# Kernel tuning notes

Measured on AMD Instinct MI355X. Metric: run time of the kernel, lower is better.

## Reference

```python
import jax, jax.numpy as jnp
import numpy as np

N = 50000      # num_nodes
E = 800000     # num_edges
F_IN = 128     # node_features
H = 128        # hidden_channels
EPS = 1e-5     # BatchNorm eps


def setup_inputs() -> dict:
    key = jax.random.key(0)
    ks = jax.random.split(key, 6)
    x = jax.random.normal(ks[0], (N, F_IN), dtype=jnp.float32)
    edge_index = jax.random.randint(ks[1], (2, E), 0, N, dtype=jnp.int64)
    s = 0.05
    return {
        "x": x,
        "edge_index": edge_index,
        "g_in": jnp.ones((F_IN,), jnp.float32),
        "be_in": jnp.zeros((F_IN,), jnp.float32),
        "w1": jax.random.normal(ks[2], (F_IN, 2 * H), jnp.float32) * s,
        "b1": jnp.zeros((2 * H,), jnp.float32),
        "g1": jnp.ones((2 * H,), jnp.float32),
        "be1": jnp.zeros((2 * H,), jnp.float32),
        "w2": jax.random.normal(ks[3], (2 * H, H), jnp.float32) * s,
        "b2": jnp.zeros((H,), jnp.float32),
        "g2": jnp.ones((H,), jnp.float32),
        "be2": jnp.zeros((H,), jnp.float32),
    }


def batchnorm(x, g, b):
    # training-mode BatchNorm1d: batch stats over the node dimension (biased var)
    m = jnp.mean(x, axis=0)
    v = jnp.var(x, axis=0)
    return (x - m) * jax.lax.rsqrt(v + EPS) * g + b


def gcn_conv(x, w, b, src, dst, deg_inv_sqrt):
    # PyG GCNConv: transform, then D^{-1/2}(A+I)D^{-1/2} aggregation, then bias
    h = x @ w                                   # [N, out]
    norm = deg_inv_sqrt[src] * deg_inv_sqrt[dst]  # [E+N]
    msg = h[src] * norm[:, None]                # gather + scale
    out = jax.ops.segment_sum(msg, dst, num_segments=N)  # scatter-add
    return out + b


def reference(x, edge_index, g_in, be_in, w1, b1, g1, be1, w2, b2, g2, be2):
    # add self-loops once
    loop = jnp.arange(N, dtype=edge_index.dtype)
    src = jnp.concatenate([edge_index[0], loop])
    dst = jnp.concatenate([edge_index[1], loop])
    deg = jax.ops.segment_sum(jnp.ones_like(src, dtype=x.dtype), dst, num_segments=N)
    deg_inv_sqrt = jnp.where(deg > 0, jax.lax.rsqrt(jnp.maximum(deg, 1.0)), 0.0)

    h = batchnorm(x, g_in, be_in)
    # layer 1: F_IN -> 2H (no residual: shapes differ); dropout is identity in eval
    h = jax.nn.relu(batchnorm(gcn_conv(h, w1, b1, src, dst, deg_inv_sqrt), g1, be1))
    # layer 2 (final): 2H -> H
    h = jax.nn.relu(batchnorm(gcn_conv(h, w2, b2, src, dst, deg_inv_sqrt), g2, be2))
    return h
```

## Files before the change

kernel.cpp:

```cpp
#include <hip/hip_runtime.h>
#include <hip/hip_bf16.h>

#define NN 50000
#define NE 800000
#define FIN 128
#define HC1 256
#define HC2 128
#define EPSV 1e-5f
#define NTILE 196
#define CAP 8448
#define FILLMAX (CAP - 3840)
#define NQ 12500
#define CELL 56

typedef __attribute__((ext_vector_type(8))) short bf8;
typedef __attribute__((ext_vector_type(16))) float f32x16;

union BF8U { bf8 v; ushort u[8]; uint4 q; };

__device__ __forceinline__ float bf2f(ushort u) {
    union { uint i; float f; } c; c.i = ((uint)u) << 16; return c.f;
}
__device__ __forceinline__ float ulo(uint u) {
    union { uint i; float f; } c; c.i = u << 16; return c.f;
}
__device__ __forceinline__ float uhi(uint u) {
    union { uint i; float f; } c; c.i = u & 0xffff0000u; return c.f;
}
__device__ __forceinline__ ushort f2bf(float f) {
    return __builtin_bit_cast(ushort, __float2bfloat16(f));
}

__global__ void k_init(float* __restrict__ stats, uint* __restrict__ s0row) {
    int i = blockIdx.x * blockDim.x + threadIdx.x;
    if (i < 1024) stats[i] = 0.0f;
    if (i < 64) s0row[i] = 0u;
}

#define BKB NTILE
#define SB 391
#define WB 128

__device__ __forceinline__ void wprep_body(const float* __restrict__ W, ushort* __restrict__ wp,
                                           int idx, int K, int NC) {
    int j = idx & 7;
    int lane = (idx >> 3) & 63;
    int ts = idx >> 9;
    int KS = K / 16;
    int s = ts % KS;
    int t = ts / KS;
    int n = t * 32 + (lane & 31);
    int k = s * 16 + (lane >> 5) * 8 + j;
    wp[idx] = f2bf(W[(size_t)k * NC + n]);
}

__global__ __launch_bounds__(256) void k_bucket(
    const int* __restrict__ ei, int* __restrict__ gcnt, uint* __restrict__ cellbuf,
    const float* __restrict__ x, float* __restrict__ sum, float* __restrict__ sumsq,
    const float* __restrict__ w1, ushort* __restrict__ wp1,
    const float* __restrict__ w2, ushort* __restrict__ wp2) {
    int b = blockIdx.x;
    int t = threadIdx.x;
    if (b < BKB) {
        __shared__ int hist[256];
        __shared__ int sscan[256];
        __shared__ int offs[256];
        __shared__ int lcur[256];
        __shared__ uint stage[4096];
        hist[t] = 0;
        __syncthreads();
        int e0 = b * 4096;
        int total = min(4096, NE - e0);
        uint eu[16];
#pragma unroll
        for (int i = 0; i < 16; ++i) {
            int e = e0 + i * 256 + t;
            if (e < NE) {
                int s = ei[e];
                int d = ei[NE + e];
                s = min(max(s, 0), NN - 1);
                d = min(max(d, 0), NN - 1);
                int tile = d >> 8;
                eu[i] = ((uint)tile << 24) | ((uint)s << 8) | (uint)(d & 255);
                atomicAdd(&hist[tile], 1);
            } else eu[i] = 0xffffffffu;
        }
        __syncthreads();
        int h = hist[t];
        sscan[t] = h;
        __syncthreads();
#pragma unroll
        for (int off = 1; off < 256; off <<= 1) {
            int v = (t >= off) ? sscan[t - off] : 0;
            __syncthreads();
            sscan[t] += v;
            __syncthreads();
        }
        int excl = sscan[t] - h;
        offs[t] = excl;
        lcur[t] = excl;
        __syncthreads();
#pragma unroll
        for (int i = 0; i < 16; ++i) {
            if (eu[i] != 0xffffffffu) {
                int tile = eu[i] >> 24;
                int p = atomicAdd(&lcur[tile], 1);
                stage[p] = eu[i];
            }
        }
        __syncthreads();
        for (int p = t; p < total; p += 256) {
            uint u = stage[p];
            int T = u >> 24;
            int idx = p - offs[T];
            if (idx < CELL) cellbuf[(size_t)T * (BKB * CELL) + b * CELL + idx] = u;
        }
        if (t < NTILE) gcnt[t * BKB + b] = hist[t];
        return;
    }
    if (b < BKB + SB) {
        const int F4 = 32, RIF = 8, RPB = 128;
        int c4 = t & 31;
        int ro = t >> 5;
        int r0 = (b - BKB) * RPB;
        int r1 = min(r0 + RPB, NN);
        float4 s = make_float4(0.f, 0.f, 0.f, 0.f);
        float4 q = make_float4(0.f, 0.f, 0.f, 0.f);
        for (int r = r0 + ro; r < r1; r += RIF) {
            float4 v = ((const float4*)x)[(size_t)r * F4 + c4];
            s.x += v.x; s.y += v.y; s.z += v.z; s.w += v.w;
            q.x += v.x * v.x; q.y += v.y * v.y; q.z += v.z * v.z; q.w += v.w * v.w;
        }
        __shared__ float4 sS[256];
        __shared__ float4 sQ[256];
        sS[t] = s; sQ[t] = q;
        __syncthreads();
#pragma unroll
        for (int st = 128; st >= 32; st >>= 1) {
            if (t < st) {
                float4 a = sS[t + st], bb = sQ[t + st];
                sS[t].x += a.x; sS[t].y += a.y; sS[t].z += a.z; sS[t].w += a.w;
                sQ[t].x += bb.x; sQ[t].y += bb.y; sQ[t].z += bb.z; sQ[t].w += bb.w;
            }
            __syncthreads();
        }
        if (t < 32) {
            float4 a = sS[t], bb = sQ[t];
            atomicAdd(&sum[t * 4 + 0], a.x); atomicAdd(&sum[t * 4 + 1], a.y);
            atomicAdd(&sum[t * 4 + 2], a.z); atomicAdd(&sum[t * 4 + 3], a.w);
            atomicAdd(&sumsq[t * 4 + 0], bb.x); atomicAdd(&sumsq[t * 4 + 1], bb.y);
            atomicAdd(&sumsq[t * 4 + 2], bb.z); atomicAdd(&sumsq[t * 4 + 3], bb.w);
        }
        return;
    }
    if (b < BKB + SB + WB) {
        wprep_body(w1, wp1, (b - BKB - SB) * 256 + t, FIN, HC1);
        return;
    }
    wprep_body(w2, wp2, (b - BKB - SB - WB) * 256 + t, HC1, HC2);
}

__global__ __launch_bounds__(256) void k_csr(
    const int* __restrict__ gcnt, const uint* __restrict__ cellbuf,
    ushort* __restrict__ csr, int* __restrict__ cnt, int* __restrict__ rowstart,
    const float* __restrict__ sumIn, const float* __restrict__ sqIn,
    const float* __restrict__ g, const float* __restrict__ be,
    const float* __restrict__ x, ushort* __restrict__ s0) {
    __shared__ uint ubuf[CAP];
    __shared__ int ccnt[256];
    __shared__ int cscan[256];
    __shared__ int cnt256[256];
    __shared__ int scan[256];
    __shared__ int offs256[256];
    __shared__ int cur256[256];
    __shared__ int dcnt[256];
    __shared__ float ssc[128];
    __shared__ float ssh[128];
    int t = threadIdx.x;
    int tile = blockIdx.x;
    int t0 = tile << 8;
    if (t < 128) {
        float mean = sumIn[t] / (float)NN;
        float var = fmaxf(sqIn[t] / (float)NN - mean * mean, 0.f);
        float s = g[t] * rsqrtf(var + EPSV);
        ssc[t] = s;
        ssh[t] = be[t] - mean * s;
    }
    int cb = (t < BKB) ? min(gcnt[tile * BKB + t], CELL) : 0;
    ccnt[t] = cb;
    cnt256[t] = 0;
    cscan[t] = cb;
    __syncthreads();
#pragma unroll
    for (int off = 1; off < 256; off <<= 1) {
        int v = (t >= off) ? cscan[t - off] : 0;
        __syncthreads();
        cscan[t] += v;
        __syncthreads();
    }
    int size = min(cscan[255], FILLMAX);
    int cexcl = cscan[t] - cb;
    for (int i = 0; i < cb; ++i) {
        int w = cexcl + i;
        if (w < size) {
            uint u = cellbuf[(size_t)tile * (BKB * CELL) + t * CELL + i] & 0x00ffffffu;
            ubuf[w] = u;
            atomicAdd(&cnt256[u & 255u], 1);
        }
    }
    __syncthreads();
    int c = cnt256[t];
    dcnt[t] = c;
    int padded = (c + 15) & ~15;
    scan[t] = padded;
    __syncthreads();
#pragma unroll
    for (int off = 1; off < 256; off <<= 1) {
        int v = (t >= off) ? scan[t - off] : 0;
        __syncthreads();
        scan[t] += v;
        __syncthreads();
    }
    int excl = scan[t] - padded;
    offs256[t] = excl;
    cur256[t] = 0;
    int r = t0 + t;
    if (r < NN) {
        cnt[r] = c;
        rowstart[r] = tile * CAP + excl;
    }
    __syncthreads();
    for (int i = t; i < size; i += 256) {
        uint u = ubuf[i];
        int l = u & 255u;
        int p = atomicAdd(&cur256[l], 1);
        int w = offs256[l] + p;
        if (w < CAP) csr[(size_t)tile * CAP + w] = (ushort)(u >> 8);
    }
    if (r < NN) {
        for (int p = c; p < padded; ++p) {
            int w = excl + p;
            if (w < CAP) csr[(size_t)tile * CAP + w] = (ushort)NN;
        }
    }
    {
        int c4 = t & 31;
        float4 sc = *(const float4*)&ssc[c4 * 4];
        float4 sh = *(const float4*)&ssh[c4 * 4];
        for (int rr = t >> 5; rr < 256; rr += 8) {
            int row = t0 + rr;
            if (row >= NN) break;
            float d = rsqrtf((float)(dcnt[rr] + 1));
            float4 v = ((const float4*)x)[(size_t)row * 32 + c4];
            ushort4 o;
            o.x = f2bf((v.x * sc.x + sh.x) * d);
            o.y = f2bf((v.y * sc.y + sh.y) * d);
            o.z = f2bf((v.z * sc.z + sh.z) * d);
            o.w = f2bf((v.w * sc.w + sh.w) * d);
            ((ushort4*)s0)[(size_t)row * 32 + c4] = o;
        }
    }
}

template<int STATS>
__global__ __launch_bounds__(256) void k_gather(
    const int* __restrict__ cnt, const int* __restrict__ rowstart,
    const ushort* __restrict__ csr, const ushort* __restrict__ src,
    ushort* __restrict__ agg, const float* __restrict__ b2,
    float* __restrict__ sum, float* __restrict__ sumsq) {
    __shared__ float lsum[128];
    __shared__ float lsq[128];
    int tid = threadIdx.x;
    int wid = tid >> 6;
    int lane = tid & 63;
    float bb0 = 0.f, bb1 = 0.f, fs0 = 0.f, fq0 = 0.f, fs1 = 0.f, fq1 = 0.f;
    if (STATS) {
        if (tid < 128) { lsum[tid] = 0.f; lsq[tid] = 0.f; }
        bb0 = b2[2 * lane];
        bb1 = b2[2 * lane + 1];
        __syncthreads();
    }
    const uint* sp = (const uint*)src;
    for (int q = blockIdx.x; q < NQ; q += gridDim.x) {
        int r = q * 4 + wid;
        int deg = cnt[r];
        int padded = (deg + 15) & ~15;
        int base = rowstart[r];
        uint v = sp[(size_t)r * 64 + lane];
        float a0 = ulo(v), a1 = uhi(v);
        for (int j = 0; j < padded; j += 16) {
            const ushort* p = csr + base + j;
            uint4 q0 = *(const uint4*)p;
            uint4 q1 = *(const uint4*)(p + 8);
            uint id[16];
            id[0]  = q0.x & 0xffffu; id[1]  = q0.x >> 16;
            id[2]  = q0.y & 0xffffu; id[3]  = q0.y >> 16;
            id[4]  = q0.z & 0xffffu; id[5]  = q0.z >> 16;
            id[6]  = q0.w & 0xffffu; id[7]  = q0.w >> 16;
            id[8]  = q1.x & 0xffffu; id[9]  = q1.x >> 16;
            id[10] = q1.y & 0xffffu; id[11] = q1.y >> 16;
            id[12] = q1.z & 0xffffu; id[13] = q1.z >> 16;
            id[14] = q1.w & 0xffffu; id[15] = q1.w >> 16;
#pragma unroll
            for (int k = 0; k < 16; ++k) id[k] = min(id[k], (uint)NN);
            uint vv[16];
#pragma unroll
            for (int k = 0; k < 16; ++k) vv[k] = sp[(size_t)id[k] * 64 + lane];
#pragma unroll
            for (int k = 0; k < 16; ++k) { a0 += ulo(vv[k]); a1 += uhi(vv[k]); }
        }
        float d = rsqrtf((float)(deg + 1));
        float a0f = a0 * d, a1f = a1 * d;
        if (STATS) {
            float v0 = a0f + bb0, v1 = a1f + bb1;
            fs0 += v0; fq0 += v0 * v0;
            fs1 += v1; fq1 += v1 * v1;
        }
        uint o = ((uint)f2bf(a1f) << 16) | (uint)f2bf(a0f);
        ((uint*)agg)[(size_t)r * 64 + lane] = o;
    }
    if (STATS) {
        atomicAdd(&lsum[2 * lane], fs0);
        atomicAdd(&lsum[2 * lane + 1], fs1);
        atomicAdd(&lsq[2 * lane], fq0);
        atomicAdd(&lsq[2 * lane + 1], fq1);
        __syncthreads();
        if (tid < 128) {
            atomicAdd(&sum[tid], lsum[tid]);
            atomicAdd(&sumsq[tid], lsq[tid]);
        }
    }
}

__global__ __launch_bounds__(256) void k_mm1(
    const ushort* __restrict__ Abf,
    const ushort* __restrict__ wp,
    const float* __restrict__ bias,
    ushort* __restrict__ Y,
    float* __restrict__ sum, float* __restrict__ sumsq)
{
    const int K = 128, NC = 256, KS = K / 16, NT = NC / 32;
    int tid = threadIdx.x;
    int wid = tid >> 6;
    int lane = tid & 63;
    int rbase = blockIdx.x * 128 + wid * 32;
    int arow = rbase + (lane & 31);
    int khalf = lane >> 5;

    __shared__ float lsum[NC];
    __shared__ float lsq[NC];
    lsum[tid] = 0.f; lsq[tid] = 0.f;
    __syncthreads();

    f32x16 acc[NT];
#pragma unroll
    for (int t = 0; t < NT; ++t)
#pragma unroll
        for (int i = 0; i < 16; ++i) acc[t][i] = 0.f;

    const uint4* Bq = (const uint4*)wp;
    const uint4* Aq = (const uint4*)Abf;
#pragma unroll
    for (int s = 0; s < KS; ++s) {
        BF8U au;
        if (arow < NN) au.q = Aq[(size_t)arow * (K / 8) + s * 2 + khalf];
        else au.q = make_uint4(0, 0, 0, 0);
#pragma unroll
        for (int t = 0; t < NT; ++t) {
            BF8U bu;
            bu.q = Bq[(t * KS + s) * 64 + lane];
            acc[t] = __builtin_amdgcn_mfma_f32_32x32x16_bf16(au.v, bu.v, acc[t], 0, 0, 0);
        }
    }

#pragma unroll
    for (int t = 0; t < NT; ++t) {
        int col = t * 32 + (lane & 31);
        float bv = bias[col];
        float fs = 0.f, fq = 0.f;
#pragma unroll
        for (int q = 0; q < 4; ++q) {
#pragma unroll
            for (int i = 0; i < 4; ++i) {
                int r = rbase + q * 8 + khalf * 4 + i;
                if (r < NN) {
                    float v = acc[t][q * 4 + i] + bv;
                    Y[(size_t)r * NC + col] = f2bf(v);
                    fs += v; fq += v * v;
                }
            }
        }
        atomicAdd(&lsum[col], fs);
        atomicAdd(&lsq[col], fq);
    }
    __syncthreads();
    atomicAdd(&sum[tid], lsum[tid]);
    atomicAdd(&sumsq[tid], lsq[tid]);
}

__global__ __launch_bounds__(256) void k_mm2(
    const ushort* __restrict__ Y,
    const ushort* __restrict__ wp,
    const float* __restrict__ sum1, const float* __restrict__ sq1,
    const float* __restrict__ g1, const float* __restrict__ be1,
    const int* __restrict__ cnt,
    ushort* __restrict__ S2)
{
    const int K = 256, NC = 128, KS = K / 16, NT = NC / 32;
    __shared__ float ssc[K];
    __shared__ float ssh[K];
    {
        int c = threadIdx.x;
        float mean = sum1[c] / (float)NN;
        float var = fmaxf(sq1[c] / (float)NN - mean * mean, 0.f);
        float s = g1[c] * rsqrtf(var + EPSV);
        ssc[c] = s;
        ssh[c] = be1[c] - mean * s;
    }
    __syncthreads();

    int wid = threadIdx.x >> 6;
    int lane = threadIdx.x & 63;
    int rbase = blockIdx.x * 128 + wid * 32;
    int arow = rbase + (lane & 31);
    int khalf = lane >> 5;

    f32x16 acc[NT];
#pragma unroll
    for (int t = 0; t < NT; ++t)
#pragma unroll
        for (int i = 0; i < 16; ++i) acc[t][i] = 0.f;

    const uint4* Bq = (const uint4*)wp;
#pragma unroll
    for (int s = 0; s < KS; ++s) {
        int k0 = s * 16 + khalf * 8;
        BF8U au;
        if (arow < NN) {
            uint4 y = *(const uint4*)&Y[(size_t)arow * K + k0];
            float4 c0 = *(const float4*)&ssc[k0];
            float4 c1 = *(const float4*)&ssc[k0 + 4];
            float4 h0 = *(const float4*)&ssh[k0];
            float4 h1 = *(const float4*)&ssh[k0 + 4];
            au.u[0] = f2bf(fmaxf(bf2f((ushort)(y.x & 0xffffu)) * c0.x + h0.x, 0.f));
            au.u[1] = f2bf(fmaxf(bf2f((ushort)(y.x >> 16))     * c0.y + h0.y, 0.f));
            au.u[2] = f2bf(fmaxf(bf2f((ushort)(y.y & 0xffffu)) * c0.z + h0.z, 0.f));
            au.u[3] = f2bf(fmaxf(bf2f((ushort)(y.y >> 16))     * c0.w + h0.w, 0.f));
            au.u[4] = f2bf(fmaxf(bf2f((ushort)(y.z & 0xffffu)) * c1.x + h1.x, 0.f));
            au.u[5] = f2bf(fmaxf(bf2f((ushort)(y.z >> 16))     * c1.y + h1.y, 0.f));
            au.u[6] = f2bf(fmaxf(bf2f((ushort)(y.w & 0xffffu)) * c1.z + h1.z, 0.f));
            au.u[7] = f2bf(fmaxf(bf2f((ushort)(y.w >> 16))     * c1.w + h1.w, 0.f));
        } else {
            au.q = make_uint4(0, 0, 0, 0);
        }
#pragma unroll
        for (int t = 0; t < NT; ++t) {
            BF8U bu;
            bu.q = Bq[(t * KS + s) * 64 + lane];
            acc[t] = __builtin_amdgcn_mfma_f32_32x32x16_bf16(au.v, bu.v, acc[t], 0, 0, 0);
        }
    }

#pragma unroll
    for (int q = 0; q < 4; ++q) {
#pragma unroll
        for (int i = 0; i < 4; ++i) {
            int r = rbase + q * 8 + khalf * 4 + i;
            if (r < NN) {
                float dv = rsqrtf((float)(cnt[r] + 1));
#pragma unroll
                for (int t = 0; t < NT; ++t) {
                    int col = t * 32 + (lane & 31);
                    S2[(size_t)r * NC + col] = f2bf(acc[t][q * 4 + i] * dv);
                }
            }
        }
    }
}

__global__ void k_bnrelu(const ushort* __restrict__ agg2, const float* __restrict__ b2,
                         const float* __restrict__ sum, const float* __restrict__ sumsq,
                         const float* __restrict__ g, const float* __restrict__ be,
                         float* __restrict__ out) {
    int idx = blockIdx.x * blockDim.x + threadIdx.x;
    const int total = NN * HC2 / 4;
    if (idx >= total) return;
    int c4 = idx & 31;
    float4 sm = ((const float4*)sum)[c4];
    float4 sq = ((const float4*)sumsq)[c4];
    float4 gg = ((const float4*)g)[c4];
    float4 bee = ((const float4*)be)[c4];
    float4 bb = ((const float4*)b2)[c4];
    float4 mean, sc, sh;
    mean.x = sm.x / (float)NN; mean.y = sm.y / (float)NN;
    mean.z = sm.z / (float)NN; mean.w = sm.w / (float)NN;
    sc.x = gg.x * rsqrtf(fmaxf(sq.x / (float)NN - mean.x * mean.x, 0.f) + EPSV);
    sc.y = gg.y * rsqrtf(fmaxf(sq.y / (float)NN - mean.y * mean.y, 0.f) + EPSV);
    sc.z = gg.z * rsqrtf(fmaxf(sq.z / (float)NN - mean.z * mean.z, 0.f) + EPSV);
    sc.w = gg.w * rsqrtf(fmaxf(sq.w / (float)NN - mean.w * mean.w, 0.f) + EPSV);
    sh.x = bee.x - mean.x * sc.x; sh.y = bee.y - mean.y * sc.y;
    sh.z = bee.z - mean.z * sc.z; sh.w = bee.w - mean.w * sc.w;
    ushort4 u = ((const ushort4*)agg2)[idx];
    float4 v;
    v.x = fmaxf((bf2f(u.x) + bb.x) * sc.x + sh.x, 0.f);
    v.y = fmaxf((bf2f(u.y) + bb.y) * sc.y + sh.y, 0.f);
    v.z = fmaxf((bf2f(u.z) + bb.z) * sc.z + sh.z, 0.f);
    v.w = fmaxf((bf2f(u.w) + bb.w) * sc.w + sh.w, 0.f);
    ((float4*)out)[idx] = v;
}

extern "C" void kernel_launch(void* const* d_in, const int* in_sizes, int n_in,
                              void* d_out, int out_size, void* d_ws, size_t ws_size,
                              hipStream_t stream) {
    const float* x     = (const float*)d_in[0];
    const int*   ei    = (const int*)d_in[1];
    const float* g_in  = (const float*)d_in[2];
    const float* be_in = (const float*)d_in[3];
    const float* w1    = (const float*)d_in[4];
    const float* b1    = (const float*)d_in[5];
    const float* g1    = (const float*)d_in[6];
    const float* be1   = (const float*)d_in[7];
    const float* w2    = (const float*)d_in[8];
    const float* b2    = (const float*)d_in[9];
    const float* g2    = (const float*)d_in[10];
    const float* be2   = (const float*)d_in[11];
    float* out = (float*)d_out;

    float* ws = (float*)d_ws;
    float* stats = ws;
    float* sumIn = stats;        float* sqIn = stats + 128;
    float* sum1  = stats + 256;  float* sq1  = stats + 512;
    float* sum2  = stats + 768;  float* sq2  = stats + 896;
    ushort* wp1   = (ushort*)(ws + 2048);
    ushort* wp2   = (ushort*)(ws + 18432);
    ushort* y1u   = (ushort*)(ws + 34816);
    ushort* s0bf  = (ushort*)(ws + 6434816);
    ushort* aggbf = (ushort*)(ws + 9634880);
    int* cnt      = (int*)(ws + 12834880);
    int* rowstart = (int*)(ws + 12884880);
    int* gcnt     = (int*)(ws + 12934880);
    uint* cellbuf = (uint*)(ws + 12973296);
    ushort* csr   = (ushort*)(ws + 15124592);

    const int sblocks = (NN + 127) / 128;

    hipLaunchKernelGGL(k_init, dim3(4), dim3(256), 0, stream,
                       stats, (uint*)s0bf + (size_t)NN * 64);

    hipLaunchKernelGGL(k_bucket, dim3(BKB + SB + 2 * WB), dim3(256), 0, stream,
                       ei, gcnt, cellbuf, x, sumIn, sqIn, w1, wp1, w2, wp2);

    hipLaunchKernelGGL(k_csr, dim3(NTILE), dim3(256), 0, stream,
                       gcnt, cellbuf, csr, cnt, rowstart,
                       sumIn, sqIn, g_in, be_in, x, s0bf);

    hipLaunchKernelGGL(k_gather<0>, dim3(NQ), dim3(256), 0, stream,
                       cnt, rowstart, csr, s0bf, aggbf, nullptr, nullptr, nullptr);

    hipLaunchKernelGGL(k_mm1, dim3(sblocks), dim3(256), 0, stream, aggbf, wp1, b1, y1u, sum1, sq1);

    hipLaunchKernelGGL(k_mm2, dim3(sblocks), dim3(256), 0, stream,
                       y1u, wp2, sum1, sq1, g1, be1, cnt, s0bf);

    hipLaunchKernelGGL(k_gather<1>, dim3(784), dim3(256), 0, stream,
                       cnt, rowstart, csr, s0bf, aggbf, b2, sum2, sq2);

    hipLaunchKernelGGL(k_bnrelu, dim3((NN * 32 + 255) / 256), dim3(256), 0, stream,
                       aggbf, b2, sum2, sq2, g2, be2, out);
}
```

Before: 231.9 us.

## Fuse layer-1 neighbor gather into the first MFMA matmul kernel, halve bucket chunks

The first-layer neighbor aggregation is merged into the first matmul. Each block gathers and normalizes 128 rows into swizzled shared memory and then runs the bf16 MFMA GEMM from there, so the aggregated intermediate never goes through global memory and one launch is removed. The edge bucketing now uses 392 blocks of 2048 edges with smaller per-cell capacity, and the CSR builder reads two cells per thread. Risks are lower occupancy and less gather parallelism in the fused kernel, since each wave serially gathers 32 rows, and possible edge truncation with the smaller CELL of 36.

```diff
diff --git a/kernel.cpp b/kernel.cpp
--- a/kernel.cpp
+++ b/kernel.cpp
@@ -11,7 +11,8 @@
 #define CAP 8448
 #define FILLMAX (CAP - 3840)
 #define NQ 12500
-#define CELL 56
+#define BKB 392
+#define CELL 36
 
 typedef __attribute__((ext_vector_type(8))) short bf8;
 typedef __attribute__((ext_vector_type(16))) float f32x16;
@@ -37,7 +38,6 @@
     if (i < 64) s0row[i] = 0u;
 }
 
-#define BKB NTILE
 #define SB 391
 #define WB 128
 
@@ -66,14 +66,14 @@
         __shared__ int sscan[256];
         __shared__ int offs[256];
         __shared__ int lcur[256];
-        __shared__ uint stage[4096];
+        __shared__ uint stage[2048];
         hist[t] = 0;
         __syncthreads();
-        int e0 = b * 4096;
-        int total = min(4096, NE - e0);
-        uint eu[16];
-#pragma unroll
-        for (int i = 0; i < 16; ++i) {
+        int e0 = b * 2048;
+        int total = min(2048, NE - e0);
+        uint eu[8];
+#pragma unroll
+        for (int i = 0; i < 8; ++i) {
             int e = e0 + i * 256 + t;
             if (e < NE) {
                 int s = ei[e];
@@ -101,7 +101,7 @@
         lcur[t] = excl;
         __syncthreads();
 #pragma unroll
-        for (int i = 0; i < 16; ++i) {
+        for (int i = 0; i < 8; ++i) {
             if (eu[i] != 0xffffffffu) {
                 int tile = eu[i] >> 24;
                 int p = atomicAdd(&lcur[tile], 1);
@@ -167,7 +167,6 @@
     const float* __restrict__ g, const float* __restrict__ be,
     const float* __restrict__ x, ushort* __restrict__ s0) {
     __shared__ uint ubuf[CAP];
-    __shared__ int ccnt[256];
     __shared__ int cscan[256];
     __shared__ int cnt256[256];
     __shared__ int scan[256];
@@ -186,10 +185,14 @@
         ssc[t] = s;
         ssh[t] = be[t] - mean * s;
     }
-    int cb = (t < BKB) ? min(gcnt[tile * BKB + t], CELL) : 0;
-    ccnt[t] = cb;
+    int cb0 = 0, cb1 = 0;
+    if (t < 196) {
+        cb0 = min(gcnt[tile * BKB + 2 * t], CELL);
+        cb1 = min(gcnt[tile * BKB + 2 * t + 1], CELL);
+    }
+    int pairsum = cb0 + cb1;
     cnt256[t] = 0;
-    cscan[t] = cb;
+    cscan[t] = pairsum;
     __syncthreads();
 #pragma unroll
     for (int off = 1; off < 256; off <<= 1) {
@@ -199,11 +202,20 @@
         __syncthreads();
     }
     int size = min(cscan[255], FILLMAX);
-    int cexcl = cscan[t] - cb;
-    for (int i = 0; i < cb; ++i) {
-        int w = cexcl + i;
+    int cexcl0 = cscan[t] - pairsum;
+    int cexcl1 = cexcl0 + cb0;
+    for (int i = 0; i < cb0; ++i) {
+        int w = cexcl0 + i;
         if (w < size) {
-            uint u = cellbuf[(size_t)tile * (BKB * CELL) + t * CELL + i] & 0x00ffffffu;
+            uint u = cellbuf[(size_t)tile * (BKB * CELL) + (2 * t) * CELL + i] & 0x00ffffffu;
+            ubuf[w] = u;
+            atomicAdd(&cnt256[u & 255u], 1);
+        }
+    }
+    for (int i = 0; i < cb1; ++i) {
+        int w = cexcl1 + i;
+        if (w < size) {
+            uint u = cellbuf[(size_t)tile * (BKB * CELL) + (2 * t + 1) * CELL + i] & 0x00ffffffu;
             ubuf[w] = u;
             atomicAdd(&cnt256[u & 255u], 1);
         }
@@ -258,6 +270,192 @@
             o.z = f2bf((v.z * sc.z + sh.z) * d);
             o.w = f2bf((v.w * sc.w + sh.w) * d);
             ((ushort4*)s0)[(size_t)row * 32 + c4] = o;
+        }
+    }
+}
+
+__global__ __launch_bounds__(256) void k_gmm1(
+    const int* __restrict__ cnt, const int* __restrict__ rowstart,
+    const ushort* __restrict__ csr, const ushort* __restrict__ src,
+    const ushort* __restrict__ wp,
+    const float* __restrict__ bias,
+    ushort* __restrict__ Y,
+    float* __restrict__ sum, float* __restrict__ sumsq)
+{
+    const int K = 128, NC = 256, KS = K / 16, NT = NC / 32;
+    __shared__ uint sAw[8192];
+    __shared__ float lsum[NC];
+    __shared__ float lsq[NC];
+    int tid = threadIdx.x;
+    int wid = tid >> 6;
+    int lane = tid & 63;
+    int rbase = blockIdx.x * 128;
+    lsum[tid] = 0.f; lsq[tid] = 0.f;
+
+    const uint* sp = (const uint*)src;
+    for (int rr = 0; rr < 32; ++rr) {
+        int rl = wid * 32 + rr;
+        int r = rbase + rl;
+        uint o = 0u;
+        if (r < NN) {
+            int deg = cnt[r];
+            int padded = (deg + 15) & ~15;
+            int base = rowstart[r];
+            uint v = sp[(size_t)r * 64 + lane];
+            float a0 = ulo(v), a1 = uhi(v);
+            for (int j = 0; j < padded; j += 16) {
+                const ushort* p = csr + base + j;
+                uint4 q0 = *(const uint4*)p;
+                uint4 q1 = *(const uint4*)(p + 8);
+                uint id[16];
+                id[0]  = q0.x & 0xffffu; id[1]  = q0.x >> 16;
+                id[2]  = q0.y & 0xffffu; id[3]  = q0.y >> 16;
+                id[4]  = q0.z & 0xffffu; id[5]  = q0.z >> 16;
+                id[6]  = q0.w & 0xffffu; id[7]  = q0.w >> 16;
+                id[8]  = q1.x & 0xffffu; id[9]  = q1.x >> 16;
+                id[10] = q1.y & 0xffffu; id[11] = q1.y >> 16;
+                id[12] = q1.z & 0xffffu; id[13] = q1.z >> 16;
+                id[14] = q1.w & 0xffffu; id[15] = q1.w >> 16;
+#pragma unroll
+                for (int k = 0; k < 16; ++k) id[k] = min(id[k], (uint)NN);
+                uint vv[16];
+#pragma unroll
+                for (int k = 0; k < 16; ++k) vv[k] = sp[(size_t)id[k] * 64 + lane];
+#pragma unroll
+                for (int k = 0; k < 16; ++k) { a0 += ulo(vv[k]); a1 += uhi(vv[k]); }
+            }
+            float d = rsqrtf((float)(deg + 1));
+            o = ((uint)f2bf(a1 * d) << 16) | (uint)f2bf(a0 * d);
+        }
+        sAw[rl * 64 + (lane ^ ((rl & 15) << 2))] = o;
+    }
+    __syncthreads();
+
+    int rl0 = wid * 32 + (lane & 31);
+    int khalf = lane >> 5;
+    int swz = (rl0 & 15) << 2;
+
+    f32x16 acc[NT];
+#pragma unroll
+    for (int t = 0; t < NT; ++t)
+#pragma unroll
+        for (int i = 0; i < 16; ++i) acc[t][i] = 0.f;
+
+    const uint4* Bq = (const uint4*)wp;
+#pragma unroll
+    for (int s = 0; s < KS; ++s) {
+        BF8U au;
+        au.q = *(const uint4*)&sAw[rl0 * 64 + ((s * 8 + khalf * 4) ^ swz)];
+#pragma unroll
+        for (int t = 0; t < NT; ++t) {
+            BF8U bu;
+            bu.q = Bq[(t * KS + s) * 64 + lane];
+            acc[t] = __builtin_amdgcn_mfma_f32_32x32x16_bf16(au.v, bu.v, acc[t], 0, 0, 0);
+        }
+    }
+
+    int rbw = rbase + wid * 32;
+#pragma unroll
+    for (int t = 0; t < NT; ++t) {
+        int col = t * 32 + (lane & 31);
+        float bv = bias[col];
+        float fs = 0.f, fq = 0.f;
+#pragma unroll
+        for (int q = 0; q < 4; ++q) {
+#pragma unroll
+            for (int i = 0; i < 4; ++i) {
+                int r = rbw + q * 8 + khalf * 4 + i;
+                if (r < NN) {
+                    float v = acc[t][q * 4 + i] + bv;
+                    Y[(size_t)r * NC + col] = f2bf(v);
+                    fs += v; fq += v * v;
+                }
+            }
+        }
+        atomicAdd(&lsum[col], fs);
+        atomicAdd(&lsq[col], fq);
+    }
+    __syncthreads();
+    atomicAdd(&sum[tid], lsum[tid]);
+    atomicAdd(&sumsq[tid], lsq[tid]);
+}
+
+__global__ __launch_bounds__(256) void k_mm2(
+    const ushort* __restrict__ Y,
+    const ushort* __restrict__ wp,
+    const float* __restrict__ sum1, const float* __restrict__ sq1,
+    const float* __restrict__ g1, const float* __restrict__ be1,
+    const int* __restrict__ cnt,
+    ushort* __restrict__ S2)
+{
+    const int K = 256, NC = 128, KS = K / 16, NT = NC / 32;
+    __shared__ float ssc[K];
+    __shared__ float ssh[K];
+    {
+        int c = threadIdx.x;
+        float mean = sum1[c] / (float)NN;
+        float var = fmaxf(sq1[c] / (float)NN - mean * mean, 0.f);
+        float s = g1[c] * rsqrtf(var + EPSV);
+        ssc[c] = s;
+        ssh[c] = be1[c] - mean * s;
+    }
+    __syncthreads();
+
+    int wid = threadIdx.x >> 6;
+    int lane = threadIdx.x & 63;
+    int rbase = blockIdx.x * 128 + wid * 32;
+    int arow = rbase + (lane & 31);
+    int khalf = lane >> 5;
+
+    f32x16 acc[NT];
+#pragma unroll
+    for (int t = 0; t < NT; ++t)
+#pragma unroll
+        for (int i = 0; i < 16; ++i) acc[t][i] = 0.f;
+
+    const uint4* Bq = (const uint4*)wp;
+#pragma unroll
+    for (int s = 0; s < KS; ++s) {
+        int k0 = s * 16 + khalf * 8;
+        BF8U au;
+        if (arow < NN) {
+            uint4 y = *(const uint4*)&Y[(size_t)arow * K + k0];
+            float4 c0 = *(const float4*)&ssc[k0];
+            float4 c1 = *(const float4*)&ssc[k0 + 4];
+            float4 h0 = *(const float4*)&ssh[k0];
+            float4 h1 = *(const float4*)&ssh[k0 + 4];
+            au.u[0] = f2bf(fmaxf(bf2f((ushort)(y.x & 0xffffu)) * c0.x + h0.x, 0.f));
+            au.u[1] = f2bf(fmaxf(bf2f((ushort)(y.x >> 16))     * c0.y + h0.y, 0.f));
+            au.u[2] = f2bf(fmaxf(bf2f((ushort)(y.y & 0xffffu)) * c0.z + h0.z, 0.f));
+            au.u[3] = f2bf(fmaxf(bf2f((ushort)(y.y >> 16))     * c0.w + h0.w, 0.f));
+            au.u[4] = f2bf(fmaxf(bf2f((ushort)(y.z & 0xffffu)) * c1.x + h1.x, 0.f));
+            au.u[5] = f2bf(fmaxf(bf2f((ushort)(y.z >> 16))     * c1.y + h1.y, 0.f));
+            au.u[6] = f2bf(fmaxf(bf2f((ushort)(y.w & 0xffffu)) * c1.z + h1.z, 0.f));
+            au.u[7] = f2bf(fmaxf(bf2f((ushort)(y.w >> 16))     * c1.w + h1.w, 0.f));
+        } else {
+            au.q = make_uint4(0, 0, 0, 0);
+        }
+#pragma unroll
+        for (int t = 0; t < NT; ++t) {
+            BF8U bu;
+            bu.q = Bq[(t * KS + s) * 64 + lane];
+            acc[t] = __builtin_amdgcn_mfma_f32_32x32x16_bf16(au.v, bu.v, acc[t], 0, 0, 0);
+        }
+    }
+
+#pragma unroll
+    for (int q = 0; q < 4; ++q) {
+#pragma unroll
+        for (int i = 0; i < 4; ++i) {
+            int r = rbase + q * 8 + khalf * 4 + i;
+            if (r < NN) {
+                float dv = rsqrtf((float)(cnt[r] + 1));
+#pragma unroll
+                for (int t = 0; t < NT; ++t) {
+                    int col = t * 32 + (lane & 31);
+                    S2[(size_t)r * NC + col] = f2bf(acc[t][q * 4 + i] * dv);
+                }
+            }
         }
     }
 }
@@ -328,152 +526,6 @@
         if (tid < 128) {
             atomicAdd(&sum[tid], lsum[tid]);
             atomicAdd(&sumsq[tid], lsq[tid]);
-        }
-    }
-}
-
-__global__ __launch_bounds__(256) void k_mm1(
-    const ushort* __restrict__ Abf,
-    const ushort* __restrict__ wp,
-    const float* __restrict__ bias,
-    ushort* __restrict__ Y,
-    float* __restrict__ sum, float* __restrict__ sumsq)
-{
-    const int K = 128, NC = 256, KS = K / 16, NT = NC / 32;
-    int tid = threadIdx.x;
-    int wid = tid >> 6;
-    int lane = tid & 63;
-    int rbase = blockIdx.x * 128 + wid * 32;
-    int arow = rbase + (lane & 31);
-    int khalf = lane >> 5;
-
-    __shared__ float lsum[NC];
-    __shared__ float lsq[NC];
-    lsum[tid] = 0.f; lsq[tid] = 0.f;
-    __syncthreads();
-
-    f32x16 acc[NT];
-#pragma unroll
-    for (int t = 0; t < NT; ++t)
-#pragma unroll
-        for (int i = 0; i < 16; ++i) acc[t][i] = 0.f;
-
-    const uint4* Bq = (const uint4*)wp;
-    const uint4* Aq = (const uint4*)Abf;
-#pragma unroll
-    for (int s = 0; s < KS; ++s) {
-        BF8U au;
-        if (arow < NN) au.q = Aq[(size_t)arow * (K / 8) + s * 2 + khalf];
-        else au.q = make_uint4(0, 0, 0, 0);
-#pragma unroll
-        for (int t = 0; t < NT; ++t) {
-            BF8U bu;
-            bu.q = Bq[(t * KS + s) * 64 + lane];
-            acc[t] = __builtin_amdgcn_mfma_f32_32x32x16_bf16(au.v, bu.v, acc[t], 0, 0, 0);
-        }
-    }
-
-#pragma unroll
-    for (int t = 0; t < NT; ++t) {
-        int col = t * 32 + (lane & 31);
-        float bv = bias[col];
-        float fs = 0.f, fq = 0.f;
-#pragma unroll
-        for (int q = 0; q < 4; ++q) {
-#pragma unroll
-            for (int i = 0; i < 4; ++i) {
-                int r = rbase + q * 8 + khalf * 4 + i;
-                if (r < NN) {
-                    float v = acc[t][q * 4 + i] + bv;
-                    Y[(size_t)r * NC + col] = f2bf(v);
-                    fs += v; fq += v * v;
-                }
-            }
-        }
-        atomicAdd(&lsum[col], fs);
-        atomicAdd(&lsq[col], fq);
-    }
-    __syncthreads();
-    atomicAdd(&sum[tid], lsum[tid]);
-    atomicAdd(&sumsq[tid], lsq[tid]);
-}
-
-__global__ __launch_bounds__(256) void k_mm2(
-    const ushort* __restrict__ Y,
-    const ushort* __restrict__ wp,
-    const float* __restrict__ sum1, const float* __restrict__ sq1,
-    const float* __restrict__ g1, const float* __restrict__ be1,
-    const int* __restrict__ cnt,
-    ushort* __restrict__ S2)
-{
-    const int K = 256, NC = 128, KS = K / 16, NT = NC / 32;
-    __shared__ float ssc[K];
-    __shared__ float ssh[K];
-    {
-        int c = threadIdx.x;
-        float mean = sum1[c] / (float)NN;
-        float var = fmaxf(sq1[c] / (float)NN - mean * mean, 0.f);
-        float s = g1[c] * rsqrtf(var + EPSV);
-        ssc[c] = s;
-        ssh[c] = be1[c] - mean * s;
-    }
-    __syncthreads();
-
-    int wid = threadIdx.x >> 6;
-    int lane = threadIdx.x & 63;
-    int rbase = blockIdx.x * 128 + wid * 32;
-    int arow = rbase + (lane & 31);
-    int khalf = lane >> 5;
-
-    f32x16 acc[NT];
-#pragma unroll
-    for (int t = 0; t < NT; ++t)
-#pragma unroll
-        for (int i = 0; i < 16; ++i) acc[t][i] = 0.f;
-
-    const uint4* Bq = (const uint4*)wp;
-#pragma unroll
-    for (int s = 0; s < KS; ++s) {
-        int k0 = s * 16 + khalf * 8;
-        BF8U au;
-        if (arow < NN) {
-            uint4 y = *(const uint4*)&Y[(size_t)arow * K + k0];
-            float4 c0 = *(const float4*)&ssc[k0];
-            float4 c1 = *(const float4*)&ssc[k0 + 4];
-            float4 h0 = *(const float4*)&ssh[k0];
-            float4 h1 = *(const float4*)&ssh[k0 + 4];
-            au.u[0] = f2bf(fmaxf(bf2f((ushort)(y.x & 0xffffu)) * c0.x + h0.x, 0.f));
-            au.u[1] = f2bf(fmaxf(bf2f((ushort)(y.x >> 16))     * c0.y + h0.y, 0.f));
-            au.u[2] = f2bf(fmaxf(bf2f((ushort)(y.y & 0xffffu)) * c0.z + h0.z, 0.f));
-            au.u[3] = f2bf(fmaxf(bf2f((ushort)(y.y >> 16))     * c0.w + h0.w, 0.f));
-            au.u[4] = f2bf(fmaxf(bf2f((ushort)(y.z & 0xffffu)) * c1.x + h1.x, 0.f));
-            au.u[5] = f2bf(fmaxf(bf2f((ushort)(y.z >> 16))     * c1.y + h1.y, 0.f));
-            au.u[6] = f2bf(fmaxf(bf2f((ushort)(y.w & 0xffffu)) * c1.z + h1.z, 0.f));
-            au.u[7] = f2bf(fmaxf(bf2f((ushort)(y.w >> 16))     * c1.w + h1.w, 0.f));
-        } else {
-            au.q = make_uint4(0, 0, 0, 0);
-        }
-#pragma unroll
-        for (int t = 0; t < NT; ++t) {
-            BF8U bu;
-            bu.q = Bq[(t * KS + s) * 64 + lane];
-            acc[t] = __builtin_amdgcn_mfma_f32_32x32x16_bf16(au.v, bu.v, acc[t], 0, 0, 0);
-        }
-    }
-
-#pragma unroll
-    for (int q = 0; q < 4; ++q) {
-#pragma unroll
-        for (int i = 0; i < 4; ++i) {
-            int r = rbase + q * 8 + khalf * 4 + i;
-            if (r < NN) {
-                float dv = rsqrtf((float)(cnt[r] + 1));
-#pragma unroll
-                for (int t = 0; t < NT; ++t) {
-                    int col = t * 32 + (lane & 31);
-                    S2[(size_t)r * NC + col] = f2bf(acc[t][q * 4 + i] * dv);
-                }
-            }
         }
     }
 }
@@ -539,8 +591,8 @@
     int* cnt      = (int*)(ws + 12834880);
     int* rowstart = (int*)(ws + 12884880);
     int* gcnt     = (int*)(ws + 12934880);
-    uint* cellbuf = (uint*)(ws + 12973296);
-    ushort* csr   = (ushort*)(ws + 15124592);
+    uint* cellbuf = (uint*)(ws + 13011712);
+    ushort* csr   = (ushort*)(ws + 15777664);
 
     const int sblocks = (NN + 127) / 128;
 
@@ -554,10 +606,8 @@
                        gcnt, cellbuf, csr, cnt, rowstart,
                        sumIn, sqIn, g_in, be_in, x, s0bf);
 
-    hipLaunchKernelGGL(k_gather<0>, dim3(NQ), dim3(256), 0, stream,
-                       cnt, rowstart, csr, s0bf, aggbf, nullptr, nullptr, nullptr);
-
-    hipLaunchKernelGGL(k_mm1, dim3(sblocks), dim3(256), 0, stream, aggbf, wp1, b1, y1u, sum1, sq1);
+    hipLaunchKernelGGL(k_gmm1, dim3(sblocks), dim3(256), 0, stream,
+                       cnt, rowstart, csr, s0bf, wp1, b1, y1u, sum1, sq1);
 
     hipLaunchKernelGGL(k_mm2, dim3(sblocks), dim3(256), 0, stream,
                        y1u, wp2, sum1, sq1, g1, be1, cnt, s0bf);
```

After: 248.9 us. 1.07x slower.

## Simplify edge bucketing to direct atomic cell writes with smaller chunks

Applied to the files above, without the earlier changes.

The edge bucketing kernel now uses twice as many blocks, each handling 2048 edges. Each edge claims a slot in its destination-tile cell with a shared atomic and writes straight to global memory, replacing the histogram, prefix scan and LDS staging pass. The CSR kernel reads two cells per thread to cover the larger block count, and the cell capacity shrinks to 36. Global writes are no longer grouped contiguously by tile, and the fixed cell cap could drop edges if a tile/chunk pair overflows it.

```diff
diff --git a/kernel.cpp b/kernel.cpp
--- a/kernel.cpp
+++ b/kernel.cpp
@@ -11,7 +11,8 @@
 #define CAP 8448
 #define FILLMAX (CAP - 3840)
 #define NQ 12500
-#define CELL 56
+#define BKB 392
+#define CELL 36
 
 typedef __attribute__((ext_vector_type(8))) short bf8;
 typedef __attribute__((ext_vector_type(16))) float f32x16;
@@ -37,7 +38,6 @@
     if (i < 64) s0row[i] = 0u;
 }
 
-#define BKB NTILE
 #define SB 391
 #define WB 128
 
@@ -62,18 +62,12 @@
     int b = blockIdx.x;
     int t = threadIdx.x;
     if (b < BKB) {
-        __shared__ int hist[256];
-        __shared__ int sscan[256];
-        __shared__ int offs[256];
         __shared__ int lcur[256];
-        __shared__ uint stage[4096];
-        hist[t] = 0;
-        __syncthreads();
-        int e0 = b * 4096;
-        int total = min(4096, NE - e0);
-        uint eu[16];
-#pragma unroll
-        for (int i = 0; i < 16; ++i) {
+        lcur[t] = 0;
+        __syncthreads();
+        int e0 = b * 2048;
+#pragma unroll
+        for (int i = 0; i < 8; ++i) {
             int e = e0 + i * 256 + t;
             if (e < NE) {
                 int s = ei[e];
@@ -81,41 +75,14 @@
                 s = min(max(s, 0), NN - 1);
                 d = min(max(d, 0), NN - 1);
                 int tile = d >> 8;
-                eu[i] = ((uint)tile << 24) | ((uint)s << 8) | (uint)(d & 255);
-                atomicAdd(&hist[tile], 1);
-            } else eu[i] = 0xffffffffu;
-        }
-        __syncthreads();
-        int h = hist[t];
-        sscan[t] = h;
-        __syncthreads();
-#pragma unroll
-        for (int off = 1; off < 256; off <<= 1) {
-            int v = (t >= off) ? sscan[t - off] : 0;
-            __syncthreads();
-            sscan[t] += v;
-            __syncthreads();
-        }
-        int excl = sscan[t] - h;
-        offs[t] = excl;
-        lcur[t] = excl;
-        __syncthreads();
-#pragma unroll
-        for (int i = 0; i < 16; ++i) {
-            if (eu[i] != 0xffffffffu) {
-                int tile = eu[i] >> 24;
                 int p = atomicAdd(&lcur[tile], 1);
-                stage[p] = eu[i];
+                if (p < CELL)
+                    cellbuf[(size_t)tile * (BKB * CELL) + b * CELL + p] =
+                        ((uint)s << 8) | (uint)(d & 255);
             }
         }
         __syncthreads();
-        for (int p = t; p < total; p += 256) {
-            uint u = stage[p];
-            int T = u >> 24;
-            int idx = p - offs[T];
-            if (idx < CELL) cellbuf[(size_t)T * (BKB * CELL) + b * CELL + idx] = u;
-        }
-        if (t < NTILE) gcnt[t * BKB + b] = hist[t];
+        if (t < NTILE) gcnt[t * BKB + b] = lcur[t];
         return;
     }
     if (b < BKB + SB) {
@@ -167,7 +134,6 @@
     const float* __restrict__ g, const float* __restrict__ be,
     const float* __restrict__ x, ushort* __restrict__ s0) {
     __shared__ uint ubuf[CAP];
-    __shared__ int ccnt[256];
     __shared__ int cscan[256];
     __shared__ int cnt256[256];
     __shared__ int scan[256];
@@ -186,10 +152,14 @@
         ssc[t] = s;
         ssh[t] = be[t] - mean * s;
     }
-    int cb = (t < BKB) ? min(gcnt[tile * BKB + t], CELL) : 0;
-    ccnt[t] = cb;
+    int cb0 = 0, cb1 = 0;
+    if (t < 196) {
+        cb0 = min(gcnt[tile * BKB + 2 * t], CELL);
+        cb1 = min(gcnt[tile * BKB + 2 * t + 1], CELL);
+    }
+    int pairsum = cb0 + cb1;
     cnt256[t] = 0;
-    cscan[t] = cb;
+    cscan[t] = pairsum;
     __syncthreads();
 #pragma unroll
     for (int off = 1; off < 256; off <<= 1) {
@@ -199,11 +169,20 @@
         __syncthreads();
     }
     int size = min(cscan[255], FILLMAX);
-    int cexcl = cscan[t] - cb;
-    for (int i = 0; i < cb; ++i) {
-        int w = cexcl + i;
+    int cexcl0 = cscan[t] - pairsum;
+    int cexcl1 = cexcl0 + cb0;
+    for (int i = 0; i < cb0; ++i) {
+        int w = cexcl0 + i;
         if (w < size) {
-            uint u = cellbuf[(size_t)tile * (BKB * CELL) + t * CELL + i] & 0x00ffffffu;
+            uint u = cellbuf[(size_t)tile * (BKB * CELL) + (2 * t) * CELL + i] & 0x00ffffffu;
+            ubuf[w] = u;
+            atomicAdd(&cnt256[u & 255u], 1);
+        }
+    }
+    for (int i = 0; i < cb1; ++i) {
+        int w = cexcl1 + i;
+        if (w < size) {
+            uint u = cellbuf[(size_t)tile * (BKB * CELL) + (2 * t + 1) * CELL + i] & 0x00ffffffu;
             ubuf[w] = u;
             atomicAdd(&cnt256[u & 255u], 1);
         }
@@ -539,8 +518,8 @@
     int* cnt      = (int*)(ws + 12834880);
     int* rowstart = (int*)(ws + 12884880);
     int* gcnt     = (int*)(ws + 12934880);
-    uint* cellbuf = (uint*)(ws + 12973296);
-    ushort* csr   = (ushort*)(ws + 15124592);
+    uint* cellbuf = (uint*)(ws + 13011712);
+    ushort* csr   = (ushort*)(ws + 15777664);
 
     const int sblocks = (NN + 127) / 128;
 
```

Measured after the change: 232.3 us. About the same (+0.2%).
